# Kernel optimization log

Measured on AMD Instinct MI355X. Metric: run time of the kernel, lower is better.

Reference implementation:

```python
import jax, jax.numpy as jnp
import numpy as np

B, T, H, OUT = 2048, 512, 256, 512


def setup_inputs() -> dict:
    key = jax.random.key(0)
    ks = jax.random.split(key, 7)
    s = 1.0 / np.sqrt(H)  # PyTorch LSTM/Linear default uniform bound
    u = lambda k, shape: jax.random.uniform(k, shape, jnp.float32, -s, s)
    return {
        "x": jax.random.normal(ks[0], (B, T, 1), jnp.float32),
        "W_ih": u(ks[1], (4 * H, 1)),
        "W_hh": u(ks[2], (4 * H, H)),
        "b_ih": u(ks[3], (4 * H,)),
        "b_hh": u(ks[4], (4 * H,)),
        "W_lin": u(ks[5], (OUT, H)),
        "b_lin": u(ks[6], (OUT,)),
    }


def reference(x, W_ih, W_hh, b_ih, b_hh, W_lin, b_lin):
    # x: [B, T, 1]. Precompute input projection for all timesteps: [B, T, 4H]
    b, t = x.shape[0], x.shape[1]
    h = W_hh.shape[1]
    x_proj = jnp.einsum('bti,gi->btg', x, W_ih) + (b_ih + b_hh)

    def step(carry, xt):  # xt: [B, 4H]
        h_prev, c_prev = carry
        gates = xt + h_prev @ W_hh.T  # [B, 4H]
        i, f, g, o = jnp.split(gates, 4, axis=-1)  # PyTorch gate order i,f,g,o
        i = jax.nn.sigmoid(i)
        f = jax.nn.sigmoid(f)
        g = jnp.tanh(g)
        o = jax.nn.sigmoid(o)
        c = f * c_prev + i * g
        h_new = o * jnp.tanh(c)
        return (h_new, c), None

    init = (jnp.zeros((b, h), x.dtype), jnp.zeros((b, h), x.dtype))
    xs = jnp.swapaxes(x_proj, 0, 1)  # [T, B, 4H]
    (h_last, _), _ = jax.lax.scan(step, init, xs)

    # Dropout(0.2) is identity in eval mode; last-step slice == final hidden state.
    return h_last @ W_lin.T + b_lin  # [B, OUT]
```

## Files before the change

### kernel.cpp

```cpp
#include <hip/hip_runtime.h>
#include <cstdint>

typedef _Float16 half8 __attribute__((ext_vector_type(8)));
typedef float floatx4 __attribute__((ext_vector_type(4)));
typedef unsigned long long u64;
typedef unsigned int u32;
typedef unsigned short u16;

#define NB 2048
#define NT 512
#define NH 256
#define NOUT 512

#define LOG2E 1.4426950408889634f
#define TWOL  2.8853900817779268f

__device__ __forceinline__ float fexp2(float x){ return __builtin_amdgcn_exp2f(x); }
__device__ __forceinline__ float frcp(float x){ return __builtin_amdgcn_rcpf(x); }

__device__ __forceinline__ floatx4 mfma16(half8 a, half8 b, floatx4 c) {
    return __builtin_amdgcn_mfma_f32_16x16x32_f16(a, b, c, 0, 0, 0);
}

__global__ void setup_kernel(const float* __restrict__ Whh, const float* __restrict__ Wlin,
                             _Float16* __restrict__ Wpack, _Float16* __restrict__ WlinPack)
{
    const int i = blockIdx.x * blockDim.x + threadIdx.x;
    const int stride = gridDim.x * blockDim.x;
    for (int k = i; k < 1024 * 256; k += stride) Wpack[k]    = (_Float16)Whh[k];
    for (int k = i; k < 512 * 256;  k += stride) WlinPack[k] = (_Float16)Wlin[k];
}

__global__ void transpose_kernel(const float* __restrict__ x, float* __restrict__ xT)
{
    __shared__ float tile[32][33];
    const int tx = threadIdx.x & 31, ty = threadIdx.x >> 5;
    const int t0 = blockIdx.x * 32;
    const int b0 = blockIdx.y * 32;
    #pragma unroll
    for (int i = 0; i < 4; i++)
        tile[ty + 8 * i][tx] = x[(size_t)(b0 + ty + 8 * i) * NT + t0 + tx];
    __syncthreads();
    #pragma unroll
    for (int i = 0; i < 4; i++)
        xT[(size_t)(t0 + ty + 8 * i) * NB + b0 + tx] = tile[tx][ty + 8 * i];
}

__global__ __launch_bounds__(512, 1)
void lstm_kernel(const float* __restrict__ xT, const float* __restrict__ Wih,
                 const float* __restrict__ bih, const float* __restrict__ bhh,
                 const _Float16* __restrict__ Wpack, u16* __restrict__ hlast)
{
    __shared__ __align__(16) u16 wlds[16][4096];
    __shared__ __align__(16) u16 hlds[2][4096];
    __shared__ float2 bwlds[1024];

    const int tid  = threadIdx.x;
    const int lane = tid & 63;
    const int wv   = tid >> 6;
    const int l15  = lane & 15;
    const int l4   = lane >> 4;
    const int r0   = blockIdx.x * 16;
    const int u0   = wv * 32;

    for (int g = tid; g < 1024; g += 512) bwlds[g] = make_float2(bih[g] + bhh[g], Wih[g]);
    for (int i = tid; i < 1024; i += 512) ((u64*)hlds[0])[i] = 0;

    for (int ch = tid; ch < 8192; ch += 512) {
        const int tl = ch >> 9;
        const int cc = ch & 511;
        const int row = cc >> 5;
        const int kch = cc & 31;
        const int G  = 768 + (tl >> 1) * 32 + (tl & 1) * 16 + row;
        half8 v = *(const half8*)(Wpack + (size_t)G * NH + kch * 8);
        *(half8*)(&wlds[tl][kch * 128 + row * 8]) = v;
    }

    half8 wreg[2][3][8];
    #pragma unroll
    for (int ug = 0; ug < 2; ug++)
        #pragma unroll
        for (int q = 0; q < 3; q++) {
            const int G = q * 256 + u0 + ug * 16 + l15;
            #pragma unroll
            for (int kc = 0; kc < 8; kc++)
                wreg[ug][q][kc] = *(const half8*)(Wpack + (size_t)G * NH + kc * 32 + l4 * 8);
        }

    float cst[8];
    #pragma unroll
    for (int i = 0; i < 8; i++) cst[i] = 0.f;

    __syncthreads();

    for (int t = 0; t < NT; t++) {
        const u16* hsrc = hlds[t & 1];
        u16*       hdst = hlds[(t + 1) & 1];
        const floatx4 xv = *(const floatx4*)(xT + (size_t)t * NB + r0 + l4 * 4);

        #pragma unroll
        for (int ug = 0; ug < 2; ug++) {
            floatx4 acc[4];
            #pragma unroll
            for (int q = 0; q < 4; q++)
                acc[q] = (floatx4){0.f, 0.f, 0.f, 0.f};

            __builtin_amdgcn_s_setprio(1);
            #pragma unroll
            for (int half_ = 0; half_ < 2; half_++) {
                half8 a[4];
                #pragma unroll
                for (int k2 = 0; k2 < 4; k2++) {
                    const int kc = half_ * 4 + k2;
                    a[k2] = *(const half8*)(hsrc + (kc * 4 + l4) * 128 + l15 * 8);
                }
                #pragma unroll
                for (int k2 = 0; k2 < 4; k2++) {
                    const int kc = half_ * 4 + k2;
                    acc[0] = mfma16(a[k2], wreg[ug][0][kc], acc[0]);
                    acc[1] = mfma16(a[k2], wreg[ug][1][kc], acc[1]);
                    acc[2] = mfma16(a[k2], wreg[ug][2][kc], acc[2]);
                    const half8 b3 = *(const half8*)(&wlds[wv * 2 + ug][(kc * 4 + l4) * 128 + l15 * 8]);
                    acc[3] = mfma16(a[k2], b3, acc[3]);
                }
            }
            __builtin_amdgcn_s_setprio(0);

            float2 bw[4];
            #pragma unroll
            for (int q = 0; q < 4; q++) bw[q] = bwlds[q * 256 + u0 + ug * 16 + l15];

            #pragma unroll
            for (int j = 0; j < 4; j++) {
                const float pi = acc[0][j] + bw[0].x + xv[j] * bw[0].y;
                const float pf = acc[1][j] + bw[1].x + xv[j] * bw[1].y;
                const float pg = acc[2][j] + bw[2].x + xv[j] * bw[2].y;
                const float po = acc[3][j] + bw[3].x + xv[j] * bw[3].y;
                const float ei = fexp2(-LOG2E * pi);
                const float ef = fexp2(-LOG2E * pf);
                const float eo = fexp2(-LOG2E * po);
                const float eg = fexp2(TWOL * pg);
                const float f  = frcp(1.f + ef);
                const float ig = (eg - 1.f) * frcp((eg + 1.f) * (1.f + ei));
                const float cc = f * cst[ug * 4 + j] + ig;
                cst[ug * 4 + j] = cc;
                const float ec = fexp2(fminf(TWOL * cc, 126.f));
                const float h  = (ec - 1.f) * frcp((ec + 1.f) * (1.f + eo));
                const int row  = l4 * 4 + j;
                const int unit = u0 + ug * 16 + l15;
                const u16 hb = __builtin_bit_cast(u16, (_Float16)h);
                const u32 ob = (u16)__shfl_xor((int)hb, 1, 64);
                if ((l15 & 1) == 0) {
                    const u32 packed = (u32)hb | (ob << 16);
                    const int idx = (unit >> 3) * 128 + row * 8 + (unit & 6);
                    *(u32*)(&hdst[idx]) = packed;
                }
            }
        }
        __syncthreads();
    }

    for (int i = tid; i < 4096; i += 512) {
        const int row = i >> 8, unit = i & 255;
        hlast[(size_t)(r0 + row) * NH + unit] =
            hlds[0][(unit >> 3) * 128 + row * 8 + (unit & 7)];
    }
}

__global__ __launch_bounds__(256, 2)
void linear_kernel(const u16* __restrict__ hlast_u, const _Float16* __restrict__ WlinPack,
                   const float* __restrict__ blin, float* __restrict__ out)
{
    const int tid = threadIdx.x;
    const int lane = tid & 63;
    const int wv = tid >> 6;
    const int mi = wv >> 1, ni = wv & 1;
    const int l15 = lane & 15, l4 = lane >> 4;
    const int r0 = (blockIdx.x >> 3) * 32;
    const int o0 = (blockIdx.x & 7) * 64;
    const _Float16* hl = (const _Float16*)hlast_u;
    const int arow = r0 + mi * 16 + l15;

    half8 a[8];
    #pragma unroll
    for (int kc = 0; kc < 8; kc++)
        a[kc] = *(const half8*)(hl + (size_t)arow * NH + kc * 32 + l4 * 8);

    #pragma unroll
    for (int nt = 0; nt < 2; nt++) {
        const int col = o0 + ni * 32 + nt * 16 + l15;
        floatx4 acc = (floatx4){0.f, 0.f, 0.f, 0.f};
        #pragma unroll
        for (int kc = 0; kc < 8; kc++) {
            const half8 b = *(const half8*)(WlinPack + (size_t)col * NH + kc * 32 + l4 * 8);
            acc = mfma16(a[kc], b, acc);
        }
        const float bb = blin[col];
        #pragma unroll
        for (int j = 0; j < 4; j++) {
            const int row = r0 + mi * 16 + l4 * 4 + j;
            out[(size_t)row * NOUT + col] = acc[j] + bb;
        }
    }
}

extern "C" void kernel_launch(void* const* d_in, const int* in_sizes, int n_in,
                              void* d_out, int out_size, void* d_ws, size_t ws_size,
                              hipStream_t stream)
{
    const float* x    = (const float*)d_in[0];
    const float* Wih  = (const float*)d_in[1];
    const float* Whh  = (const float*)d_in[2];
    const float* bih  = (const float*)d_in[3];
    const float* bhh  = (const float*)d_in[4];
    const float* Wlin = (const float*)d_in[5];
    const float* blin = (const float*)d_in[6];

    char* ws = (char*)d_ws;
    _Float16* Wpack    = (_Float16*)(ws);
    _Float16* WlinPack = (_Float16*)(ws + (512 << 10));
    u16*      hlast    = (u16*)(ws + (768 << 10));
    float*    xT       = (float*)d_out;

    setup_kernel<<<256, 256, 0, stream>>>(Whh, Wlin, Wpack, WlinPack);
    transpose_kernel<<<dim3(16, 64), 256, 0, stream>>>(x, xT);
    lstm_kernel<<<128, 512, 0, stream>>>(xT, Wih, bih, bhh, Wpack, hlast);
    linear_kernel<<<512, 256, 0, stream>>>(hlast, WlinPack, blin, (float*)d_out);
}
```

Measured before the change: 1.273 ms.

## Merge prep kernels and fuse final linear layer into LSTM kernel epilogue

Result: no change. 1.286 ms (+1.0%).

```diff
diff --git a/kernel.cpp b/kernel.cpp
--- a/kernel.cpp
+++ b/kernel.cpp
@@ -22,34 +22,38 @@
     return __builtin_amdgcn_mfma_f32_16x16x32_f16(a, b, c, 0, 0, 0);
 }
 
-__global__ void setup_kernel(const float* __restrict__ Whh, const float* __restrict__ Wlin,
-                             _Float16* __restrict__ Wpack, _Float16* __restrict__ WlinPack)
-{
-    const int i = blockIdx.x * blockDim.x + threadIdx.x;
-    const int stride = gridDim.x * blockDim.x;
-    for (int k = i; k < 1024 * 256; k += stride) Wpack[k]    = (_Float16)Whh[k];
-    for (int k = i; k < 512 * 256;  k += stride) WlinPack[k] = (_Float16)Wlin[k];
-}
-
-__global__ void transpose_kernel(const float* __restrict__ x, float* __restrict__ xT)
-{
-    __shared__ float tile[32][33];
-    const int tx = threadIdx.x & 31, ty = threadIdx.x >> 5;
-    const int t0 = blockIdx.x * 32;
-    const int b0 = blockIdx.y * 32;
-    #pragma unroll
-    for (int i = 0; i < 4; i++)
-        tile[ty + 8 * i][tx] = x[(size_t)(b0 + ty + 8 * i) * NT + t0 + tx];
-    __syncthreads();
-    #pragma unroll
-    for (int i = 0; i < 4; i++)
-        xT[(size_t)(t0 + ty + 8 * i) * NB + b0 + tx] = tile[tx][ty + 8 * i];
-}
-
+__global__ void prep_kernel(const float* __restrict__ x, const float* __restrict__ Whh,
+                            const float* __restrict__ Wlin, _Float16* __restrict__ Wpack,
+                            _Float16* __restrict__ WlinPack, float* __restrict__ xT)
+{
+    const int b = blockIdx.x;
+    if (b < 1024) {
+        __shared__ float tile[32][33];
+        const int tx = threadIdx.x & 31, ty = threadIdx.x >> 5;
+        const int t0 = (b & 15) * 32;
+        const int b0 = (b >> 4) * 32;
+        #pragma unroll
+        for (int i = 0; i < 4; i++)
+            tile[ty + 8 * i][tx] = x[(size_t)(b0 + ty + 8 * i) * NT + t0 + tx];
+        __syncthreads();
+        #pragma unroll
+        for (int i = 0; i < 4; i++)
+            xT[(size_t)(t0 + ty + 8 * i) * NB + b0 + tx] = tile[tx][ty + 8 * i];
+    } else {
+        const int i = (b - 1024) * 256 + threadIdx.x;
+        const int stride = 256 * 256;
+        for (int k = i; k < 1024 * 256; k += stride) Wpack[k]    = (_Float16)Whh[k];
+        for (int k = i; k < 512 * 256;  k += stride) WlinPack[k] = (_Float16)Wlin[k];
+    }
+}
+
+template<int FUSED>
 __global__ __launch_bounds__(512, 1)
 void lstm_kernel(const float* __restrict__ xT, const float* __restrict__ Wih,
                  const float* __restrict__ bih, const float* __restrict__ bhh,
-                 const _Float16* __restrict__ Wpack, u16* __restrict__ hlast)
+                 const _Float16* __restrict__ Wpack, const _Float16* __restrict__ WlinPack,
+                 const float* __restrict__ blin, float* __restrict__ outp,
+                 u16* __restrict__ hlast)
 {
     __shared__ __align__(16) u16 wlds[16][4096];
     __shared__ __align__(16) u16 hlds[2][4096];
@@ -98,6 +102,11 @@
         u16*       hdst = hlds[(t + 1) & 1];
         const floatx4 xv = *(const floatx4*)(xT + (size_t)t * NB + r0 + l4 * 4);
 
+        half8 aL[4];
+        #pragma unroll
+        for (int k2 = 0; k2 < 4; k2++)
+            aL[k2] = *(const half8*)(hsrc + (k2 * 4 + l4) * 128 + l15 * 8);
+
         #pragma unroll
         for (int ug = 0; ug < 2; ug++) {
             floatx4 acc[4];
@@ -107,22 +116,26 @@
 
             __builtin_amdgcn_s_setprio(1);
             #pragma unroll
-            for (int half_ = 0; half_ < 2; half_++) {
-                half8 a[4];
-                #pragma unroll
-                for (int k2 = 0; k2 < 4; k2++) {
-                    const int kc = half_ * 4 + k2;
-                    a[k2] = *(const half8*)(hsrc + (kc * 4 + l4) * 128 + l15 * 8);
-                }
-                #pragma unroll
-                for (int k2 = 0; k2 < 4; k2++) {
-                    const int kc = half_ * 4 + k2;
-                    acc[0] = mfma16(a[k2], wreg[ug][0][kc], acc[0]);
-                    acc[1] = mfma16(a[k2], wreg[ug][1][kc], acc[1]);
-                    acc[2] = mfma16(a[k2], wreg[ug][2][kc], acc[2]);
-                    const half8 b3 = *(const half8*)(&wlds[wv * 2 + ug][(kc * 4 + l4) * 128 + l15 * 8]);
-                    acc[3] = mfma16(a[k2], b3, acc[3]);
-                }
+            for (int k2 = 0; k2 < 4; k2++) {
+                const int kc = k2;
+                acc[0] = mfma16(aL[k2], wreg[ug][0][kc], acc[0]);
+                acc[1] = mfma16(aL[k2], wreg[ug][1][kc], acc[1]);
+                acc[2] = mfma16(aL[k2], wreg[ug][2][kc], acc[2]);
+                const half8 b3 = *(const half8*)(&wlds[wv * 2 + ug][(kc * 4 + l4) * 128 + l15 * 8]);
+                acc[3] = mfma16(aL[k2], b3, acc[3]);
+            }
+            half8 aH[4];
+            #pragma unroll
+            for (int k2 = 0; k2 < 4; k2++)
+                aH[k2] = *(const half8*)(hsrc + ((k2 + 4) * 4 + l4) * 128 + l15 * 8);
+            #pragma unroll
+            for (int k2 = 0; k2 < 4; k2++) {
+                const int kc = k2 + 4;
+                acc[0] = mfma16(aH[k2], wreg[ug][0][kc], acc[0]);
+                acc[1] = mfma16(aH[k2], wreg[ug][1][kc], acc[1]);
+                acc[2] = mfma16(aH[k2], wreg[ug][2][kc], acc[2]);
+                const half8 b3 = *(const half8*)(&wlds[wv * 2 + ug][(kc * 4 + l4) * 128 + l15 * 8]);
+                acc[3] = mfma16(aH[k2], b3, acc[3]);
             }
             __builtin_amdgcn_s_setprio(0);
 
@@ -160,10 +173,33 @@
         __syncthreads();
     }
 
-    for (int i = tid; i < 4096; i += 512) {
-        const int row = i >> 8, unit = i & 255;
-        hlast[(size_t)(r0 + row) * NH + unit] =
-            hlds[0][(unit >> 3) * 128 + row * 8 + (unit & 7)];
+    if constexpr (FUSED) {
+        const u16* hT = hlds[0];
+        half8 af[8];
+        #pragma unroll
+        for (int kc = 0; kc < 8; kc++)
+            af[kc] = *(const half8*)(hT + (kc * 4 + l4) * 128 + l15 * 8);
+        const int o0 = wv * 64;
+        #pragma unroll
+        for (int nt = 0; nt < 4; nt++) {
+            const int col = o0 + nt * 16 + l15;
+            floatx4 accL = (floatx4){0.f, 0.f, 0.f, 0.f};
+            #pragma unroll
+            for (int kc = 0; kc < 8; kc++) {
+                const half8 b = *(const half8*)(WlinPack + (size_t)col * NH + kc * 32 + l4 * 8);
+                accL = mfma16(af[kc], b, accL);
+            }
+            const float bb = blin[col];
+            #pragma unroll
+            for (int j = 0; j < 4; j++)
+                outp[(size_t)(r0 + l4 * 4 + j) * NOUT + col] = accL[j] + bb;
+        }
+    } else {
+        for (int i = tid; i < 4096; i += 512) {
+            const int row = i >> 8, unit = i & 255;
+            hlast[(size_t)(r0 + row) * NH + unit] =
+                hlds[0][(unit >> 3) * 128 + row * 8 + (unit & 7)];
+        }
     }
 }
 
@@ -219,11 +255,21 @@
     char* ws = (char*)d_ws;
     _Float16* Wpack    = (_Float16*)(ws);
     _Float16* WlinPack = (_Float16*)(ws + (512 << 10));
-    u16*      hlast    = (u16*)(ws + (768 << 10));
-    float*    xT       = (float*)d_out;
-
-    setup_kernel<<<256, 256, 0, stream>>>(Whh, Wlin, Wpack, WlinPack);
-    transpose_kernel<<<dim3(16, 64), 256, 0, stream>>>(x, xT);
-    lstm_kernel<<<128, 512, 0, stream>>>(xT, Wih, bih, bhh, Wpack, hlast);
-    linear_kernel<<<512, 256, 0, stream>>>(hlast, WlinPack, blin, (float*)d_out);
-}
+
+    const size_t need_fused = (768 << 10) + (size_t)NT * NB * 4;
+    const bool fused = ws_size >= need_fused;
+
+    if (fused) {
+        float* xT = (float*)(ws + (768 << 10));
+        prep_kernel<<<1280, 256, 0, stream>>>(x, Whh, Wlin, Wpack, WlinPack, xT);
+        lstm_kernel<1><<<128, 512, 0, stream>>>(xT, Wih, bih, bhh, Wpack,
+                                                WlinPack, blin, (float*)d_out, nullptr);
+    } else {
+        u16*   hlast = (u16*)(ws + (768 << 10));
+        float* xT    = (float*)d_out;
+        prep_kernel<<<1280, 256, 0, stream>>>(x, Whh, Wlin, Wpack, WlinPack, xT);
+        lstm_kernel<0><<<128, 512, 0, stream>>>(xT, Wih, bih, bhh, Wpack,
+                                                WlinPack, blin, nullptr, hlast);
+        linear_kernel<<<512, 256, 0, stream>>>(hlast, WlinPack, blin, (float*)d_out);
+    }
+}
```
